# Optimization experiments

Measured on AMD Instinct MI355X. Metric: run time of the kernel, lower is better.

## Reference

```python
import jax, jax.numpy as jnp
import numpy as np

N_NODES = 20000
N_EDGES = 640000
NODE_DIM = 128
HIDDEN = 128
NUM_LAYERS = 3


def setup_inputs() -> dict:
    key = jax.random.key(0)
    ks = jax.random.split(key, 6)
    x = jax.random.normal(ks[0], (N_NODES, NODE_DIM), dtype=jnp.float32)
    edge_index = jax.random.randint(ks[1], (2, N_EDGES), 0, N_NODES, dtype=jnp.int64)
    s = 1.0 / np.sqrt(NODE_DIM)
    W_in = jax.random.uniform(ks[2], (NODE_DIM, HIDDEN), jnp.float32, -s, s)
    b_in = jax.random.uniform(ks[3], (HIDDEN,), jnp.float32, -s, s)
    sh = 1.0 / np.sqrt(HIDDEN)
    Ws = jax.random.uniform(ks[4], (NUM_LAYERS, HIDDEN, HIDDEN), jnp.float32, -sh, sh)
    bs = jax.random.uniform(ks[5], (NUM_LAYERS, HIDDEN), jnp.float32, -sh, sh)
    return {"x": x, "edge_index": edge_index, "W_in": W_in, "b_in": b_in, "Ws": Ws, "bs": bs}


def reference(x, edge_index, W_in, b_in, Ws, bs):
    N = x.shape[0]
    loop = jnp.arange(N, dtype=edge_index.dtype)
    src = jnp.concatenate([edge_index[0], loop])  # self-loops added (PyG GCNConv default)
    dst = jnp.concatenate([edge_index[1], loop])
    # symmetric normalization: deg computed on destination nodes
    deg = jax.ops.segment_sum(jnp.ones_like(dst, dtype=x.dtype), dst, num_segments=N)
    dis = jax.lax.rsqrt(jnp.where(deg > 0, deg, 1.0))
    norm = dis[src] * dis[dst]  # [E+N]
    h = x @ W_in + b_in
    for i in range(Ws.shape[0]):
        xw = h @ Ws[i]                              # [N, H]
        msg = xw[src] * norm[:, None]               # gather + scale
        agg = jax.ops.segment_sum(msg, dst, num_segments=N) + bs[i]
        h = jax.nn.relu(agg)                        # dropout p=0 -> identity
    return h
```

## Files before the change

kernel.cpp:

```cpp
#include <hip/hip_runtime.h>
#include <hip/hip_bf16.h>


#define HDIM 128

typedef __attribute__((ext_vector_type(8))) short s8v;
typedef __attribute__((ext_vector_type(4))) float f4v;
typedef __attribute__((ext_vector_type(4))) float f4x;
typedef __attribute__((ext_vector_type(2))) uint u2x;

__device__ __forceinline__ ushort f2bf(float f) {
    uint u = __float_as_uint(f);
    u += 0x7FFFu + ((u >> 16) & 1u);
    return (ushort)(u >> 16);
}
__device__ __forceinline__ float bf2f(ushort h) {
    return __uint_as_float(((uint)h) << 16);
}
__device__ __forceinline__ void split8(float4 a, float4 b, s8v& hi, s8v& lo) {
    ushort h0 = f2bf(a.x), h1 = f2bf(a.y), h2 = f2bf(a.z), h3 = f2bf(a.w);
    ushort h4 = f2bf(b.x), h5 = f2bf(b.y), h6 = f2bf(b.z), h7 = f2bf(b.w);
    hi[0] = (short)h0; hi[1] = (short)h1; hi[2] = (short)h2; hi[3] = (short)h3;
    hi[4] = (short)h4; hi[5] = (short)h5; hi[6] = (short)h6; hi[7] = (short)h7;
    lo[0] = (short)f2bf(a.x - bf2f(h0)); lo[1] = (short)f2bf(a.y - bf2f(h1));
    lo[2] = (short)f2bf(a.z - bf2f(h2)); lo[3] = (short)f2bf(a.w - bf2f(h3));
    lo[4] = (short)f2bf(b.x - bf2f(h4)); lo[5] = (short)f2bf(b.y - bf2f(h5));
    lo[6] = (short)f2bf(b.z - bf2f(h6)); lo[7] = (short)f2bf(b.w - bf2f(h7));
}


__global__ __launch_bounds__(256) void k_count(const int* __restrict__ dst,
                                               int* __restrict__ off4,
                                               int* __restrict__ rank, int E4) {
    int t = blockIdx.x * 256 + threadIdx.x;
    if (t >= E4) return;
    int4 d = ((const int4*)dst)[t];
    int4 r;
    r.x = atomicAdd(&off4[d.x * 4 + 0], 1);
    r.y = atomicAdd(&off4[d.y * 4 + 1], 1);
    r.z = atomicAdd(&off4[d.z * 4 + 2], 1);
    r.w = atomicAdd(&off4[d.w * 4 + 3], 1);
    ((int4*)rank)[t] = r;
}

__global__ __launch_bounds__(256) void k_scan_blk(int* __restrict__ off4,
                                                  float* __restrict__ dis,
                                                  int* __restrict__ bsum, int N) {
    int t = threadIdx.x;
    int total = N * 4;
    int base = blockIdx.x * 1024 + t * 4;
    int4 d = make_int4(0, 0, 0, 0);
    if (base < total) {
        d = *(const int4*)(off4 + base);
        dis[base >> 2] = rsqrtf((float)(d.x + d.y + d.z + d.w + 1));
    }
    int tsum = d.x + d.y + d.z + d.w;
    int lane = t & 63;
    int incl = tsum;
    #pragma unroll
    for (int ofs = 1; ofs < 64; ofs <<= 1) {
        int u = __shfl_up(incl, ofs);
        if (lane >= ofs) incl += u;
    }
    __shared__ int wsum[4];
    if (lane == 63) wsum[t >> 6] = incl;
    __syncthreads();
    int w = t >> 6;
    int woff = 0;
    for (int i = 0; i < w; ++i) woff += wsum[i];

    int run = woff + incl - tsum;
    if (base < total) {
        off4[base + 0] = run; run += d.x;
        off4[base + 1] = run; run += d.y;
        off4[base + 2] = run; run += d.z;
        off4[base + 3] = run;
    }
    if (t == 255) bsum[blockIdx.x] = woff + incl;
}

__global__ __launch_bounds__(256) void k_scan_add(int* __restrict__ off4,
                                                  const int* __restrict__ bsum,
                                                  int N, int E) {
    int bid = blockIdx.x;
    if (bid == 0) {
        if (threadIdx.x == 0) off4[N * 4] = E;
        return;
    }
    int p = 0;
    for (int i = 0; i < bid; ++i) p += bsum[i];
    int base = bid * 1024 + threadIdx.x * 4;
    if (base < N * 4) {
        int4 v = *(const int4*)(off4 + base);
        v.x += p; v.y += p; v.z += p; v.w += p;
        *(int4*)(off4 + base) = v;
    }
}

__global__ __launch_bounds__(256) void k_fill(const int* __restrict__ src,
                                              const int* __restrict__ dst,
                                              const int* __restrict__ off4,
                                              const int* __restrict__ rank,
                                              int* __restrict__ csr, int E4) {
    int t = blockIdx.x * 256 + threadIdx.x;
    if (t >= E4) return;
    int4 s = ((const int4*)src)[t];
    int4 d = ((const int4*)dst)[t];
    int4 r = ((const int4*)rank)[t];
    csr[off4[d.x * 4 + 0] + r.x] = s.x;
    csr[off4[d.y * 4 + 1] + r.y] = s.y;
    csr[off4[d.z * 4 + 2] + r.z] = s.z;
    csr[off4[d.w * 4 + 3] + r.w] = s.w;
}

__global__ __launch_bounds__(256) void k_pre(const float* __restrict__ W_in,
                                             const float* __restrict__ Ws,
                                             const float* __restrict__ b_in,
                                             ushort* __restrict__ Wf,
                                             float* __restrict__ bc,
                                             int* __restrict__ off4,
                                             int N, int nbZ) {
    int bid = blockIdx.x;
    if (bid < nbZ) {
        int i = bid * 256 + threadIdx.x;
        if (i < N * 4 + 4) off4[i] = 0;
    } else if (bid < nbZ + 192) {
        int idx = (bid - nbZ) * 256 + threadIdx.x;
        int m = idx >> 14;
        int e = idx & 16383;
        int k = e >> 7, col = e & 127;
        float w;
        if (m == 0) {
            w = 0.f;
            #pragma unroll 8
            for (int j = 0; j < 128; ++j)
                w = fmaf(W_in[k * 128 + j], Ws[j * 128 + col], w);
        } else {
            w = Ws[m * 16384 + k * 128 + col];
        }
        ushort hi = f2bf(w);
        ushort lo = f2bf(w - bf2f(hi));
        int ks = k >> 5, lk = (k >> 3) & 3, j = k & 7;
        int ct = col >> 4, lane = lk * 16 + (col & 15);
        int o = m * 32768 + (ks * 8 + ct) * 512 + lane * 8 + j;
        Wf[o] = hi;
        Wf[o + 16384] = lo;
    } else {
        int col = threadIdx.x;
        if (col < 128) {
            float v = 0.f;
            #pragma unroll 8
            for (int j = 0; j < 128; ++j)
                v = fmaf(b_in[j], Ws[j * 128 + col], v);
            bc[col] = v;
        }
    }
}

template<int L0>
__global__ __launch_bounds__(256) void k_mgemm(const ushort* Ahi, const ushort* Alo,
                                               const float* __restrict__ xf,
                                               const ushort* __restrict__ Wf,
                                               const float* __restrict__ bias,
                                               const float* __restrict__ scale,
                                               ushort* xwb, int M) {
    int l = threadIdx.x & 63;
    int ch = blockIdx.x & 1;
    int strip = (blockIdx.x >> 1) * 4 + (threadIdx.x >> 6);
    int r0 = strip * 16;
    int lr = l & 15, lk = l >> 4;
    int ar = r0 + lr; if (ar >= M) ar = M - 1;

    s8v ah0, ah1, ah2, ah3, al0, al1, al2, al3;
    if (L0) {
        const float* xr = xf + (long long)ar * HDIM + lk * 8;
        split8(*(const float4*)(xr),      *(const float4*)(xr + 4),  ah0, al0);
        split8(*(const float4*)(xr + 32), *(const float4*)(xr + 36), ah1, al1);
        split8(*(const float4*)(xr + 64), *(const float4*)(xr + 68), ah2, al2);
        split8(*(const float4*)(xr + 96), *(const float4*)(xr + 100), ah3, al3);
    } else {
        ah0 = *(const s8v*)(Ahi + (long long)ar * HDIM + lk * 8);
        ah1 = *(const s8v*)(Ahi + (long long)ar * HDIM + lk * 8 + 32);
        ah2 = *(const s8v*)(Ahi + (long long)ar * HDIM + lk * 8 + 64);
        ah3 = *(const s8v*)(Ahi + (long long)ar * HDIM + lk * 8 + 96);
        al0 = *(const s8v*)(Alo + (long long)ar * HDIM + lk * 8);
        al1 = *(const s8v*)(Alo + (long long)ar * HDIM + lk * 8 + 32);
        al2 = *(const s8v*)(Alo + (long long)ar * HDIM + lk * 8 + 64);
        al3 = *(const s8v*)(Alo + (long long)ar * HDIM + lk * 8 + 96);
    }

    f4v acc[4];
    #pragma unroll
    for (int c = 0; c < 4; ++c) acc[c] = (f4v){0.f, 0.f, 0.f, 0.f};

#define KSTEP(AH, AL, ksi)                                                          \
    {                                                                               \
        const ushort* wb = Wf + ((ksi) * 8 + ch * 4) * 512 + l * 8;                 \
        _Pragma("unroll")                                                           \
        for (int c = 0; c < 4; ++c) {                                               \
            s8v bh = *(const s8v*)(wb + c * 512);                                   \
            s8v bl = *(const s8v*)(wb + 16384 + c * 512);                           \
            acc[c] = __builtin_amdgcn_mfma_f32_16x16x32_bf16(AH, bh, acc[c], 0,0,0);\
            acc[c] = __builtin_amdgcn_mfma_f32_16x16x32_bf16(AH, bl, acc[c], 0,0,0);\
            acc[c] = __builtin_amdgcn_mfma_f32_16x16x32_bf16(AL, bh, acc[c], 0,0,0);\
        }                                                                           \
    }
    KSTEP(ah0, al0, 0)
    KSTEP(ah1, al1, 1)
    KSTEP(ah2, al2, 2)
    KSTEP(ah3, al3, 3)
#undef KSTEP

    if (r0 >= M) return;
    float bbv[4], sc[4];
    #pragma unroll
    for (int c = 0; c < 4; ++c) bbv[c] = bias ? bias[(ch * 4 + c) * 16 + lr] : 0.f;
    #pragma unroll
    for (int j = 0; j < 4; ++j) sc[j] = scale[r0 + lk * 4 + j];

    #pragma unroll
    for (int c = 0; c < 4; ++c) {
        #pragma unroll
        for (int j = 0; j < 4; ++j) {
            int row = r0 + lk * 4 + j;
            if (row >= M) continue;
            float o = (acc[c][j] + bbv[c]) * sc[j];
            int cc = c * 16 + lr;
            xwb[((long long)ch * M + row) * 64 + cc] = f2bf(o);
        }
    }
}

template<int LAST>
__global__ __launch_bounds__(256) void k_agg(const int* __restrict__ off4,
                                             const int* __restrict__ csr,
                                             const float* __restrict__ dis,
                                             const ushort* __restrict__ xwb,
                                             const float* __restrict__ b,
                                             float* __restrict__ outf,
                                             ushort* __restrict__ outhi,
                                             ushort* __restrict__ outlo, int N) {
    int lane = threadIdx.x & 63;
    int wv = threadIdx.x >> 6;
    int t = lane & 15, q = lane >> 4;
    int sl = blockIdx.x & 1;
    const ushort* xs = xwb + (long long)sl * N * 64;

    int v0 = (blockIdx.x >> 1) * 4 + wv;
    int vstride = (gridDim.x >> 1) * 4;

    float4 bb = ((const float4*)(b + sl * 64))[t];

#define GATH(sidx)                                                          \
    {                                                                       \
        uint2 u = *(const uint2*)(xs + (long long)(sidx) * 64 + (t << 2));  \
        ax += bf2f((ushort)u.x); ay += bf2f((ushort)(u.x >> 16));           \
        az += bf2f((ushort)u.y); aw += bf2f((ushort)(u.y >> 16));           \
    }
#define SEL(c) (q == 0 ? (c).x : q == 1 ? (c).y : q == 2 ? (c).z : (c).w)

    for (int v = v0; v < N; v += vstride) {
        int start = off4[v << 2];
        int end   = off4[(v << 2) + 4];
        float dv = dis[v];

        float ax = 0.f, ay = 0.f, az = 0.f, aw = 0.f;
        if (q == 0) GATH(v);

        int i = start;
        for (; i + 32 <= end; i += 32) {
            int ib = __builtin_amdgcn_readfirstlane(i);
            int4 c0 = *(const int4*)(csr + ib);
            int4 c1 = *(const int4*)(csr + ib + 4);
            int4 c2 = *(const int4*)(csr + ib + 8);
            int4 c3 = *(const int4*)(csr + ib + 12);
            int4 c4 = *(const int4*)(csr + ib + 16);
            int4 c5 = *(const int4*)(csr + ib + 20);
            int4 c6 = *(const int4*)(csr + ib + 24);
            int4 c7 = *(const int4*)(csr + ib + 28);
            int s0 = SEL(c0), s1 = SEL(c1), s2 = SEL(c2), s3 = SEL(c3);
            int s4 = SEL(c4), s5 = SEL(c5), s6 = SEL(c6), s7 = SEL(c7);
            GATH(s0); GATH(s1); GATH(s2); GATH(s3);
            GATH(s4); GATH(s5); GATH(s6); GATH(s7);
        }
        if (i + 16 <= end) {
            int ib = __builtin_amdgcn_readfirstlane(i);
            int4 c0 = *(const int4*)(csr + ib);
            int4 c1 = *(const int4*)(csr + ib + 4);
            int4 c2 = *(const int4*)(csr + ib + 8);
            int4 c3 = *(const int4*)(csr + ib + 12);
            int s0 = SEL(c0), s1 = SEL(c1), s2 = SEL(c2), s3 = SEL(c3);
            GATH(s0); GATH(s1); GATH(s2); GATH(s3);
            i += 16;
        }
        if (i + 8 <= end) {
            int ib = __builtin_amdgcn_readfirstlane(i);
            int4 c0 = *(const int4*)(csr + ib);
            int4 c1 = *(const int4*)(csr + ib + 4);
            int s0 = SEL(c0), s1 = SEL(c1);
            GATH(s0); GATH(s1);
            i += 8;
        }
        if (i + 4 <= end) {
            int ib = __builtin_amdgcn_readfirstlane(i);
            int4 c0 = *(const int4*)(csr + ib);
            int s0 = SEL(c0);
            GATH(s0);
            i += 4;
        }
        {
            int r = end - i;
            if (q < r) {
                int s = csr[__builtin_amdgcn_readfirstlane(i) + q];
                GATH(s);
            }
        }

        ax += __shfl_xor(ax, 16); ax += __shfl_xor(ax, 32);
        ay += __shfl_xor(ay, 16); ay += __shfl_xor(ay, 32);
        az += __shfl_xor(az, 16); az += __shfl_xor(az, 32);
        aw += __shfl_xor(aw, 16); aw += __shfl_xor(aw, 32);

        if (q == 0) {
            float ox = fmaxf(fmaf(dv, ax, bb.x), 0.f);
            float oy = fmaxf(fmaf(dv, ay, bb.y), 0.f);
            float oz = fmaxf(fmaf(dv, az, bb.z), 0.f);
            float ow = fmaxf(fmaf(dv, aw, bb.w), 0.f);
            long long oidx = (long long)v * HDIM + sl * 64 + (t << 2);
            if (LAST) {
                f4x o4 = {ox, oy, oz, ow};
                __builtin_nontemporal_store(o4, (f4x*)(outf + oidx));
            } else {
                ushort h0 = f2bf(ox), h1 = f2bf(oy), h2 = f2bf(oz), h3 = f2bf(ow);
                u2x ph, pl;
                ph[0] = (uint)h0 | ((uint)h1 << 16);
                ph[1] = (uint)h2 | ((uint)h3 << 16);
                pl[0] = (uint)f2bf(ox - bf2f(h0)) | ((uint)f2bf(oy - bf2f(h1)) << 16);
                pl[1] = (uint)f2bf(oz - bf2f(h2)) | ((uint)f2bf(ow - bf2f(h3)) << 16);
                __builtin_nontemporal_store(ph, (u2x*)(outhi + oidx));
                __builtin_nontemporal_store(pl, (u2x*)(outlo + oidx));
            }
        }
    }
#undef GATH
#undef SEL
}

extern "C" void kernel_launch(void* const* d_in, const int* in_sizes, int n_in,
                              void* d_out, int out_size, void* d_ws, size_t ws_size,
                              hipStream_t stream) {
    const float* x    = (const float*)d_in[0];
    const int*   ei   = (const int*)d_in[1];
    const float* W_in = (const float*)d_in[2];
    const float* b_in = (const float*)d_in[3];
    const float* Ws   = (const float*)d_in[4];
    const float* bs   = (const float*)d_in[5];

    const int N = in_sizes[0] / HDIM;
    const int E = in_sizes[1] / 2;
    const int* src = ei;
    const int* dst = ei + E;

    float*  dis  = (float*)d_ws;
    int*    off4 = (int*)(dis + N);
    int*    csr  = off4 + 4 * N + 4;
    int*    rank = csr + E;
    ushort* hh   = (ushort*)(rank + E);
    ushort* hl   = hh + (long long)N * HDIM;
    ushort* xwb  = hl + (long long)N * HDIM;
    float*  bc   = (float*)(xwb + (long long)2 * N * 64);
    ushort* Wf   = (ushort*)d_out;

    int nbZ     = (4 * N + 4 + 255) / 256;
    int nb_E4   = (E / 4 + 255) / 256;
    int nb_scan = (4 * N + 1023) / 1024;
    int strips  = (N + 15) / 16;
    int nb_mg   = 2 * ((strips + 3) / 4);
    int nb_pre  = nbZ + 192 + 1;
    int nb_agg  = 2048;

    k_pre<<<nb_pre, 256, 0, stream>>>(W_in, Ws, b_in, Wf, bc, off4, N, nbZ);

    k_count   <<<nb_E4,   256, 0, stream>>>(dst, off4, rank, E / 4);
    k_scan_blk<<<nb_scan, 256, 0, stream>>>(off4, dis, csr, N);
    k_scan_add<<<nb_scan, 256, 0, stream>>>(off4, csr, N, E);
    k_fill    <<<nb_E4,   256, 0, stream>>>(src, dst, off4, rank, csr, E / 4);

    for (int layer = 0; layer < 3; ++layer) {
        const ushort* Wfm = Wf + (long long)layer * 32768;
        const float* b = bs + (long long)layer * HDIM;
        if (layer == 0)
            k_mgemm<1><<<nb_mg, 256, 0, stream>>>(nullptr, nullptr, x, Wfm,
                                                  bc, dis, xwb, N);
        else
            k_mgemm<0><<<nb_mg, 256, 0, stream>>>(hh, hl, nullptr, Wfm,
                                                  nullptr, dis, xwb, N);
        if (layer == 2)
            k_agg<1><<<nb_agg, 256, 0, stream>>>(off4, csr, dis, xwb, b,
                                                 (float*)d_out, nullptr, nullptr, N);
        else
            k_agg<0><<<nb_agg, 256, 0, stream>>>(off4, csr, dis, xwb, b,
                                                 nullptr, hh, hl, N);
    }
}
```

Measured before the change: 156.2 us.

## Merge setup kernels and fuse first GEMM with CSR fill, decoupled-lookback scan

Replaces the zeroing-in-kernel with a memset and merges weight preprocessing with the degree-count atomics in one launch. The two-pass scan becomes a single kernel where each block publishes its sum and spins on the sums of earlier blocks. The CSR fill and the layer-0 GEMM now run as disjoint block ranges of one launch. The aim is fewer launches and serialization gaps. The spin-wait scan relies on earlier blocks being scheduled before later ones, which risks stalls or deadlock.

```diff
diff --git a/kernel.cpp b/kernel.cpp
--- a/kernel.cpp
+++ b/kernel.cpp
@@ -28,104 +28,91 @@
     lo[6] = (short)f2bf(b.z - bf2f(h6)); lo[7] = (short)f2bf(b.w - bf2f(h7));
 }
 
-
-__global__ __launch_bounds__(256) void k_count(const int* __restrict__ dst,
-                                               int* __restrict__ off4,
-                                               int* __restrict__ rank, int E4) {
-    int t = blockIdx.x * 256 + threadIdx.x;
-    if (t >= E4) return;
-    int4 d = ((const int4*)dst)[t];
-    int4 r;
-    r.x = atomicAdd(&off4[d.x * 4 + 0], 1);
-    r.y = atomicAdd(&off4[d.y * 4 + 1], 1);
-    r.z = atomicAdd(&off4[d.z * 4 + 2], 1);
-    r.w = atomicAdd(&off4[d.w * 4 + 3], 1);
-    ((int4*)rank)[t] = r;
-}
-
-__global__ __launch_bounds__(256) void k_scan_blk(int* __restrict__ off4,
-                                                  float* __restrict__ dis,
-                                                  int* __restrict__ bsum, int N) {
-    int t = threadIdx.x;
-    int total = N * 4;
-    int base = blockIdx.x * 1024 + t * 4;
-    int4 d = make_int4(0, 0, 0, 0);
-    if (base < total) {
-        d = *(const int4*)(off4 + base);
-        dis[base >> 2] = rsqrtf((float)(d.x + d.y + d.z + d.w + 1));
-    }
-    int tsum = d.x + d.y + d.z + d.w;
-    int lane = t & 63;
-    int incl = tsum;
+__device__ __forceinline__ void mgemm_body(
+    int vb, int tid, bool l0,
+    const float* xf, const ushort* Ahi, const ushort* Alo,
+    const ushort* Wfm, const float* bias, const float* dis,
+    ushort* xwb, int M) {
+    int l = tid & 63;
+    int ch = vb & 1;
+    int strip = (vb >> 1) * 4 + (tid >> 6);
+    int r0 = strip * 16;
+    int lr = l & 15, lk = l >> 4;
+    int ar = r0 + lr; if (ar >= M) ar = M - 1;
+
+    s8v ah0, ah1, ah2, ah3, al0, al1, al2, al3;
+    if (l0) {
+        const float* xr = xf + (long long)ar * HDIM + lk * 8;
+        split8(*(const float4*)(xr),      *(const float4*)(xr + 4),   ah0, al0);
+        split8(*(const float4*)(xr + 32), *(const float4*)(xr + 36),  ah1, al1);
+        split8(*(const float4*)(xr + 64), *(const float4*)(xr + 68),  ah2, al2);
+        split8(*(const float4*)(xr + 96), *(const float4*)(xr + 100), ah3, al3);
+    } else {
+        ah0 = *(const s8v*)(Ahi + (long long)ar * HDIM + lk * 8);
+        ah1 = *(const s8v*)(Ahi + (long long)ar * HDIM + lk * 8 + 32);
+        ah2 = *(const s8v*)(Ahi + (long long)ar * HDIM + lk * 8 + 64);
+        ah3 = *(const s8v*)(Ahi + (long long)ar * HDIM + lk * 8 + 96);
+        al0 = *(const s8v*)(Alo + (long long)ar * HDIM + lk * 8);
+        al1 = *(const s8v*)(Alo + (long long)ar * HDIM + lk * 8 + 32);
+        al2 = *(const s8v*)(Alo + (long long)ar * HDIM + lk * 8 + 64);
+        al3 = *(const s8v*)(Alo + (long long)ar * HDIM + lk * 8 + 96);
+    }
+
+    f4v acc[4];
     #pragma unroll
-    for (int ofs = 1; ofs < 64; ofs <<= 1) {
-        int u = __shfl_up(incl, ofs);
-        if (lane >= ofs) incl += u;
-    }
-    __shared__ int wsum[4];
-    if (lane == 63) wsum[t >> 6] = incl;
-    __syncthreads();
-    int w = t >> 6;
-    int woff = 0;
-    for (int i = 0; i < w; ++i) woff += wsum[i];
-
-    int run = woff + incl - tsum;
-    if (base < total) {
-        off4[base + 0] = run; run += d.x;
-        off4[base + 1] = run; run += d.y;
-        off4[base + 2] = run; run += d.z;
-        off4[base + 3] = run;
-    }
-    if (t == 255) bsum[blockIdx.x] = woff + incl;
-}
-
-__global__ __launch_bounds__(256) void k_scan_add(int* __restrict__ off4,
-                                                  const int* __restrict__ bsum,
-                                                  int N, int E) {
+    for (int c = 0; c < 4; ++c) acc[c] = (f4v){0.f, 0.f, 0.f, 0.f};
+
+#define KSTEP(AH, AL, ksi)                                                          \
+    {                                                                               \
+        const ushort* wb = Wfm + ((ksi) * 8 + ch * 4) * 512 + l * 8;                \
+        _Pragma("unroll")                                                           \
+        for (int c = 0; c < 4; ++c) {                                               \
+            s8v bh = *(const s8v*)(wb + c * 512);                                   \
+            s8v bl = *(const s8v*)(wb + 16384 + c * 512);                           \
+            acc[c] = __builtin_amdgcn_mfma_f32_16x16x32_bf16(AH, bh, acc[c], 0,0,0);\
+            acc[c] = __builtin_amdgcn_mfma_f32_16x16x32_bf16(AH, bl, acc[c], 0,0,0);\
+            acc[c] = __builtin_amdgcn_mfma_f32_16x16x32_bf16(AL, bh, acc[c], 0,0,0);\
+        }                                                                           \
+    }
+    KSTEP(ah0, al0, 0)
+    KSTEP(ah1, al1, 1)
+    KSTEP(ah2, al2, 2)
+    KSTEP(ah3, al3, 3)
+#undef KSTEP
+
+    if (r0 < M) {
+        float bbv[4], sc[4];
+        #pragma unroll
+        for (int c = 0; c < 4; ++c)
+            bbv[c] = bias ? bias[(ch * 4 + c) * 16 + lr] : 0.f;
+        #pragma unroll
+        for (int j = 0; j < 4; ++j) {
+            int rr = r0 + lk * 4 + j;
+            sc[j] = (rr < M) ? dis[rr] : 0.f;
+        }
+        #pragma unroll
+        for (int c = 0; c < 4; ++c) {
+            #pragma unroll
+            for (int j = 0; j < 4; ++j) {
+                int row = r0 + lk * 4 + j;
+                if (row < M) {
+                    float o = (acc[c][j] + bbv[c]) * sc[j];
+                    int cc = c * 16 + lr;
+                    xwb[((long long)ch * M + row) * 64 + cc] = f2bf(o);
+                }
+            }
+        }
+    }
+}
+
+__global__ __launch_bounds__(256) void k_precount(
+    const float* __restrict__ W_in, const float* __restrict__ Ws,
+    const float* __restrict__ b_in, ushort* __restrict__ Wf,
+    float* __restrict__ bc, const int* __restrict__ dst,
+    int* __restrict__ off4, int* __restrict__ rank, int E4) {
     int bid = blockIdx.x;
-    if (bid == 0) {
-        if (threadIdx.x == 0) off4[N * 4] = E;
-        return;
-    }
-    int p = 0;
-    for (int i = 0; i < bid; ++i) p += bsum[i];
-    int base = bid * 1024 + threadIdx.x * 4;
-    if (base < N * 4) {
-        int4 v = *(const int4*)(off4 + base);
-        v.x += p; v.y += p; v.z += p; v.w += p;
-        *(int4*)(off4 + base) = v;
-    }
-}
-
-__global__ __launch_bounds__(256) void k_fill(const int* __restrict__ src,
-                                              const int* __restrict__ dst,
-                                              const int* __restrict__ off4,
-                                              const int* __restrict__ rank,
-                                              int* __restrict__ csr, int E4) {
-    int t = blockIdx.x * 256 + threadIdx.x;
-    if (t >= E4) return;
-    int4 s = ((const int4*)src)[t];
-    int4 d = ((const int4*)dst)[t];
-    int4 r = ((const int4*)rank)[t];
-    csr[off4[d.x * 4 + 0] + r.x] = s.x;
-    csr[off4[d.y * 4 + 1] + r.y] = s.y;
-    csr[off4[d.z * 4 + 2] + r.z] = s.z;
-    csr[off4[d.w * 4 + 3] + r.w] = s.w;
-}
-
-__global__ __launch_bounds__(256) void k_pre(const float* __restrict__ W_in,
-                                             const float* __restrict__ Ws,
-                                             const float* __restrict__ b_in,
-                                             ushort* __restrict__ Wf,
-                                             float* __restrict__ bc,
-                                             int* __restrict__ off4,
-                                             int N, int nbZ) {
-    int bid = blockIdx.x;
-    if (bid < nbZ) {
-        int i = bid * 256 + threadIdx.x;
-        if (i < N * 4 + 4) off4[i] = 0;
-    } else if (bid < nbZ + 192) {
-        int idx = (bid - nbZ) * 256 + threadIdx.x;
+    if (bid < 192) {
+        int idx = bid * 256 + threadIdx.x;
         int m = idx >> 14;
         int e = idx & 16383;
         int k = e >> 7, col = e & 127;
@@ -145,7 +132,7 @@
         int o = m * 32768 + (ks * 8 + ct) * 512 + lane * 8 + j;
         Wf[o] = hi;
         Wf[o + 16384] = lo;
-    } else {
+    } else if (bid == 192) {
         int col = threadIdx.x;
         if (col < 128) {
             float v = 0.f;
@@ -154,81 +141,98 @@
                 v = fmaf(b_in[j], Ws[j * 128 + col], v);
             bc[col] = v;
         }
-    }
-}
-
-template<int L0>
+    } else {
+        int t = (bid - 193) * 256 + threadIdx.x;
+        if (t >= E4) return;
+        int4 d = ((const int4*)dst)[t];
+        int4 r;
+        r.x = atomicAdd(&off4[d.x * 4 + 0], 1);
+        r.y = atomicAdd(&off4[d.y * 4 + 1], 1);
+        r.z = atomicAdd(&off4[d.z * 4 + 2], 1);
+        r.w = atomicAdd(&off4[d.w * 4 + 3], 1);
+        ((int4*)rank)[t] = r;
+    }
+}
+
+__global__ __launch_bounds__(256) void k_scan(int* __restrict__ off4,
+                                              float* __restrict__ dis,
+                                              int* bpub, int N, int E) {
+    int t = threadIdx.x;
+    int bid = blockIdx.x;
+    int total = N * 4;
+    int base = bid * 1024 + t * 4;
+    int4 d = make_int4(0, 0, 0, 0);
+    if (base < total) {
+        d = *(const int4*)(off4 + base);
+        dis[base >> 2] = rsqrtf((float)(d.x + d.y + d.z + d.w + 1));
+    }
+    int tsum = d.x + d.y + d.z + d.w;
+    int lane = t & 63;
+    int incl = tsum;
+    #pragma unroll
+    for (int ofs = 1; ofs < 64; ofs <<= 1) {
+        int u = __shfl_up(incl, ofs);
+        if (lane >= ofs) incl += u;
+    }
+    __shared__ int wsum[4];
+    if (lane == 63) wsum[t >> 6] = incl;
+    __syncthreads();
+    int w = t >> 6;
+    int woff = 0;
+    for (int i = 0; i < w; ++i) woff += wsum[i];
+
+    if (t == 255) atomicExch(&bpub[bid], (woff + incl) + 1);
+
+    __shared__ int pref;
+    if (t == 0) pref = 0;
+    __syncthreads();
+    for (int i = t; i < bid; i += 256) {
+        int v;
+        do { v = atomicAdd(&bpub[i], 0); } while (v == 0);
+        atomicAdd(&pref, v - 1);
+    }
+    __syncthreads();
+    int run = pref + woff + incl - tsum;
+
+    if (base < total) {
+        off4[base + 0] = run; run += d.x;
+        off4[base + 1] = run; run += d.y;
+        off4[base + 2] = run; run += d.z;
+        off4[base + 3] = run;
+    }
+    if (bid == 0 && t == 0) off4[N * 4] = E;
+}
+
+__global__ __launch_bounds__(256) void k_fillgemm(
+    const int* __restrict__ src, const int* __restrict__ dst,
+    const int* __restrict__ off4, const int* __restrict__ rank,
+    int* __restrict__ csr, int E4, int nbF,
+    const float* __restrict__ x, const ushort* __restrict__ Wf,
+    const float* __restrict__ bc, const float* __restrict__ dis,
+    ushort* __restrict__ xwb, int M) {
+    int bid = blockIdx.x;
+    if (bid < nbF) {
+        int t = bid * 256 + threadIdx.x;
+        if (t >= E4) return;
+        int4 s = ((const int4*)src)[t];
+        int4 d = ((const int4*)dst)[t];
+        int4 r = ((const int4*)rank)[t];
+        csr[off4[d.x * 4 + 0] + r.x] = s.x;
+        csr[off4[d.y * 4 + 1] + r.y] = s.y;
+        csr[off4[d.z * 4 + 2] + r.z] = s.z;
+        csr[off4[d.w * 4 + 3] + r.w] = s.w;
+    } else {
+        mgemm_body(bid - nbF, threadIdx.x, true, x, nullptr, nullptr,
+                   Wf, bc, dis, xwb, M);
+    }
+}
+
 __global__ __launch_bounds__(256) void k_mgemm(const ushort* Ahi, const ushort* Alo,
-                                               const float* __restrict__ xf,
                                                const ushort* __restrict__ Wf,
-                                               const float* __restrict__ bias,
-                                               const float* __restrict__ scale,
+                                               const float* __restrict__ dis,
                                                ushort* xwb, int M) {
-    int l = threadIdx.x & 63;
-    int ch = blockIdx.x & 1;
-    int strip = (blockIdx.x >> 1) * 4 + (threadIdx.x >> 6);
-    int r0 = strip * 16;
-    int lr = l & 15, lk = l >> 4;
-    int ar = r0 + lr; if (ar >= M) ar = M - 1;
-
-    s8v ah0, ah1, ah2, ah3, al0, al1, al2, al3;
-    if (L0) {
-        const float* xr = xf + (long long)ar * HDIM + lk * 8;
-        split8(*(const float4*)(xr),      *(const float4*)(xr + 4),  ah0, al0);
-        split8(*(const float4*)(xr + 32), *(const float4*)(xr + 36), ah1, al1);
-        split8(*(const float4*)(xr + 64), *(const float4*)(xr + 68), ah2, al2);
-        split8(*(const float4*)(xr + 96), *(const float4*)(xr + 100), ah3, al3);
-    } else {
-        ah0 = *(const s8v*)(Ahi + (long long)ar * HDIM + lk * 8);
-        ah1 = *(const s8v*)(Ahi + (long long)ar * HDIM + lk * 8 + 32);
-        ah2 = *(const s8v*)(Ahi + (long long)ar * HDIM + lk * 8 + 64);
-        ah3 = *(const s8v*)(Ahi + (long long)ar * HDIM + lk * 8 + 96);
-        al0 = *(const s8v*)(Alo + (long long)ar * HDIM + lk * 8);
-        al1 = *(const s8v*)(Alo + (long long)ar * HDIM + lk * 8 + 32);
-        al2 = *(const s8v*)(Alo + (long long)ar * HDIM + lk * 8 + 64);
-        al3 = *(const s8v*)(Alo + (long long)ar * HDIM + lk * 8 + 96);
-    }
-
-    f4v acc[4];
-    #pragma unroll
-    for (int c = 0; c < 4; ++c) acc[c] = (f4v){0.f, 0.f, 0.f, 0.f};
-
-#define KSTEP(AH, AL, ksi)                                                          \
-    {                                                                               \
-        const ushort* wb = Wf + ((ksi) * 8 + ch * 4) * 512 + l * 8;                 \
-        _Pragma("unroll")                                                           \
-        for (int c = 0; c < 4; ++c) {                                               \
-            s8v bh = *(const s8v*)(wb + c * 512);                                   \
-            s8v bl = *(const s8v*)(wb + 16384 + c * 512);                           \
-            acc[c] = __builtin_amdgcn_mfma_f32_16x16x32_bf16(AH, bh, acc[c], 0,0,0);\
-            acc[c] = __builtin_amdgcn_mfma_f32_16x16x32_bf16(AH, bl, acc[c], 0,0,0);\
-            acc[c] = __builtin_amdgcn_mfma_f32_16x16x32_bf16(AL, bh, acc[c], 0,0,0);\
-        }                                                                           \
-    }
-    KSTEP(ah0, al0, 0)
-    KSTEP(ah1, al1, 1)
-    KSTEP(ah2, al2, 2)
-    KSTEP(ah3, al3, 3)
-#undef KSTEP
-
-    if (r0 >= M) return;
-    float bbv[4], sc[4];
-    #pragma unroll
-    for (int c = 0; c < 4; ++c) bbv[c] = bias ? bias[(ch * 4 + c) * 16 + lr] : 0.f;
-    #pragma unroll
-    for (int j = 0; j < 4; ++j) sc[j] = scale[r0 + lk * 4 + j];
-
-    #pragma unroll
-    for (int c = 0; c < 4; ++c) {
-        #pragma unroll
-        for (int j = 0; j < 4; ++j) {
-            int row = r0 + lk * 4 + j;
-            if (row >= M) continue;
-            float o = (acc[c][j] + bbv[c]) * sc[j];
-            int cc = c * 16 + lr;
-            xwb[((long long)ch * M + row) * 64 + cc] = f2bf(o);
-        }
-    }
+    mgemm_body(blockIdx.x, threadIdx.x, false, nullptr, Ahi, Alo,
+               Wf, nullptr, dis, xwb, M);
 }
 
 template<int LAST>
@@ -363,7 +367,8 @@
 
     float*  dis  = (float*)d_ws;
     int*    off4 = (int*)(dis + N);
-    int*    csr  = off4 + 4 * N + 4;
+    int*    bpub = off4 + 4 * N + 4;
+    int*    csr  = bpub + 128;
     int*    rank = csr + E;
     ushort* hh   = (ushort*)(rank + E);
     ushort* hl   = hh + (long long)N * HDIM;
@@ -371,35 +376,27 @@
     float*  bc   = (float*)(xwb + (long long)2 * N * 64);
     ushort* Wf   = (ushort*)d_out;
 
-    int nbZ     = (4 * N + 4 + 255) / 256;
-    int nb_E4   = (E / 4 + 255) / 256;
+    int E4      = E / 4;
+    int nb_E4   = (E4 + 255) / 256;
     int nb_scan = (4 * N + 1023) / 1024;
     int strips  = (N + 15) / 16;
     int nb_mg   = 2 * ((strips + 3) / 4);
-    int nb_pre  = nbZ + 192 + 1;
     int nb_agg  = 2048;
 
-    k_pre<<<nb_pre, 256, 0, stream>>>(W_in, Ws, b_in, Wf, bc, off4, N, nbZ);
-
-    k_count   <<<nb_E4,   256, 0, stream>>>(dst, off4, rank, E / 4);
-    k_scan_blk<<<nb_scan, 256, 0, stream>>>(off4, dis, csr, N);
-    k_scan_add<<<nb_scan, 256, 0, stream>>>(off4, csr, N, E);
-    k_fill    <<<nb_E4,   256, 0, stream>>>(src, dst, off4, rank, csr, E / 4);
-
-    for (int layer = 0; layer < 3; ++layer) {
-        const ushort* Wfm = Wf + (long long)layer * 32768;
-        const float* b = bs + (long long)layer * HDIM;
-        if (layer == 0)
-            k_mgemm<1><<<nb_mg, 256, 0, stream>>>(nullptr, nullptr, x, Wfm,
-                                                  bc, dis, xwb, N);
-        else
-            k_mgemm<0><<<nb_mg, 256, 0, stream>>>(hh, hl, nullptr, Wfm,
-                                                  nullptr, dis, xwb, N);
-        if (layer == 2)
-            k_agg<1><<<nb_agg, 256, 0, stream>>>(off4, csr, dis, xwb, b,
-                                                 (float*)d_out, nullptr, nullptr, N);
-        else
-            k_agg<0><<<nb_agg, 256, 0, stream>>>(off4, csr, dis, xwb, b,
-                                                 nullptr, hh, hl, N);
-    }
-}
+    hipMemsetAsync(off4, 0, (size_t)(4 * N + 4 + 128) * sizeof(int), stream);
+
+    k_precount<<<193 + nb_E4, 256, 0, stream>>>(W_in, Ws, b_in, Wf, bc,
+                                                dst, off4, rank, E4);
+    k_scan<<<nb_scan, 256, 0, stream>>>(off4, dis, bpub, N, E);
+    k_fillgemm<<<nb_E4 + nb_mg, 256, 0, stream>>>(src, dst, off4, rank, csr,
+                                                  E4, nb_E4, x, Wf, bc, dis,
+                                                  xwb, N);
+    k_agg<0><<<nb_agg, 256, 0, stream>>>(off4, csr, dis, xwb, bs + 0 * HDIM,
+                                         nullptr, hh, hl, N);
+    k_mgemm<<<nb_mg, 256, 0, stream>>>(hh, hl, Wf + 32768, dis, xwb, N);
+    k_agg<0><<<nb_agg, 256, 0, stream>>>(off4, csr, dis, xwb, bs + 1 * HDIM,
+                                         nullptr, hh, hl, N);
+    k_mgemm<<<nb_mg, 256, 0, stream>>>(hh, hl, Wf + 65536, dis, xwb, N);
+    k_agg<1><<<nb_agg, 256, 0, stream>>>(off4, csr, dis, xwb, bs + 2 * HDIM,
+                                         (float*)d_out, nullptr, nullptr, N);
+}
```

New measurement: 156.5 us. Within noise of the previous version (+0.2%).
